# Kernel optimization log

Measured on AMD Instinct MI355X. Metric: run time of the kernel, lower is better.

Reference implementation:

```python
import jax, jax.numpy as jnp
import numpy as np

N1 = 4096
N2 = 4096


def _encoder(x, w1, b1, w2, b2, w3, b3):
    # fc1 -> fc2 -> fc3 -> relu (relu only after fc3, matching the torch code)
    h = x @ w1.T + b1
    h = h @ w2.T + b2
    h = h @ w3.T + b3
    return jax.nn.relu(h)


def _self_attention(x, adj, alpha, W):
    # tmp_i = sum_j [adj_ij==1] * alpha_ij * W * x_j ; tmp_i /= deg_i ; tmp_i += x_i (only if deg_i != 0)
    a = (adj == 1).astype(x.dtype)          # [N, N]
    deg = a.sum(axis=1)                     # [N]
    agg = (a * alpha) @ x                   # [N, 64] masked weighted aggregation
    agg = agg * W[0, 0]
    safe_deg = jnp.maximum(deg, 1.0)
    out = agg / safe_deg[:, None] + x       # residual
    return jnp.where((deg != 0.0)[:, None], out, jnp.zeros_like(out))


def setup_inputs() -> dict:
    key = jax.random.key(0)
    ks = jax.random.split(key, 20)
    s = 0.02  # weight scale to keep activations sane through the 4096->256->128->64 MLP
    inp = {
        "x1": jax.random.normal(ks[0], (N1, N1), jnp.float32),
        "x2": jax.random.normal(ks[1], (N2, N2), jnp.float32),
        "adj1": jax.random.randint(ks[2], (N1, N1), 0, 2, jnp.int32),
        "adj2": jax.random.randint(ks[3], (N2, N2), 0, 2, jnp.int32),
        "e1_w1": jax.random.normal(ks[4], (256, N1), jnp.float32) * s,
        "e1_b1": jnp.zeros((256,), jnp.float32),
        "e1_w2": jax.random.normal(ks[5], (128, 256), jnp.float32) * s,
        "e1_b2": jnp.zeros((128,), jnp.float32),
        "e1_w3": jax.random.normal(ks[6], (64, 128), jnp.float32) * s,
        "e1_b3": jnp.zeros((64,), jnp.float32),
        "e2_w1": jax.random.normal(ks[7], (256, N2), jnp.float32) * s,
        "e2_b1": jnp.zeros((256,), jnp.float32),
        "e2_w2": jax.random.normal(ks[8], (128, 256), jnp.float32) * s,
        "e2_b2": jnp.zeros((128,), jnp.float32),
        "e2_w3": jax.random.normal(ks[9], (64, 128), jnp.float32) * s,
        "e2_b3": jnp.zeros((64,), jnp.float32),
        "W": jax.random.normal(ks[10], (1, 1), jnp.float32),
        "alpha1": jax.random.normal(ks[11], (N1, N1), jnp.float32),
        "clf_w": jax.random.normal(ks[12], (2, (N1 + N2) * 64), jnp.float32) * s,
        "clf_b": jnp.zeros((2,), jnp.float32),
    }
    return inp


def reference(x1, x2, adj1, adj2,
              e1_w1, e1_b1, e1_w2, e1_b2, e1_w3, e1_b3,
              e2_w1, e2_b1, e2_w2, e2_b2, e2_w3, e2_b3,
              W, alpha1, clf_w, clf_b):
    h1 = _encoder(x1, e1_w1, e1_b1, e1_w2, e1_b2, e1_w3, e1_b3)  # [N1, 64]
    h2 = _encoder(x2, e2_w1, e2_b1, e2_w2, e2_b2, e2_w3, e2_b3)  # [N2, 64]
    # NOTE: original torch code uses self.alpha1 for BOTH graphs (alpha2 is unused)
    new1 = _self_attention(h1, adj1, alpha1, W)
    new2 = _self_attention(h2, adj2, alpha1[:N2, :N2], W)
    feat = jnp.concatenate([new1, new2], axis=0).reshape(1, -1)  # [1, (N1+N2)*64]
    return feat @ clf_w.T + clf_b  # [1, 2]
```

## Files before the change

### kernel.cpp

```cpp
#include <hip/hip_runtime.h>
#include <hip/hip_bf16.h>
#include <stdint.h>

#define N 4096

typedef __attribute__((ext_vector_type(4))) float f32x4;
typedef __attribute__((ext_vector_type(8))) short s16x8;

__device__ inline unsigned short f2bf(float f) {
    unsigned int u = __float_as_uint(f);
    u += 0x7fffu + ((u >> 16) & 1u);
    return (unsigned short)(u >> 16);
}
__device__ inline float bf2f(unsigned short h) {
    return __uint_as_float(((unsigned int)h) << 16);
}

__global__ void k0a(const float* __restrict__ w2a, const float* __restrict__ w3a,
                    const float* __restrict__ b1a, const float* __restrict__ b2a, const float* __restrict__ b3a,
                    const float* __restrict__ w2b, const float* __restrict__ w3b,
                    const float* __restrict__ b1b, const float* __restrict__ b2b, const float* __restrict__ b3b,
                    float* __restrict__ T, float* __restrict__ beff) {
    const int g  = blockIdx.x >> 5;
    const int nb = blockIdx.x & 31;
    const float* w2 = g ? w2b : w2a;
    const float* w3 = g ? w3b : w3a;
    const int c  = threadIdx.x;
    const int n0 = nb * 2;
    float a0 = 0.f, a1 = 0.f;
#pragma unroll 8
    for (int r = 0; r < 128; ++r) {
        float w = w2[r * 256 + c];
        a0 += w3[n0 * 128 + r] * w;
        a1 += w3[n0 * 128 + 128 + r] * w;
    }
    float* Tg = T + g * 64 * 256;
    Tg[n0 * 256 + c]       = a0;
    Tg[(n0 + 1) * 256 + c] = a1;

    if (nb == 0) {
        __shared__ float ps[256];
        __shared__ float u[128];
        const float* b1 = g ? b1b : b1a;
        const float* b2 = g ? b2b : b2a;
        const float* b3 = g ? b3b : b3a;
        {
            const int r = threadIdx.x >> 1, half = threadIdx.x & 1;
            float s = 0.f;
#pragma unroll 8
            for (int cc = 0; cc < 128; ++cc) s += w2[r * 256 + half * 128 + cc] * b1[half * 128 + cc];
            ps[threadIdx.x] = s;
        }
        __syncthreads();
        if (threadIdx.x < 128)
            u[threadIdx.x] = ps[2 * threadIdx.x] + ps[2 * threadIdx.x + 1] + b2[threadIdx.x];
        __syncthreads();
        {
            const int n = threadIdx.x >> 2, qr = threadIdx.x & 3;
            float s = 0.f;
#pragma unroll
            for (int r = 0; r < 32; ++r) s += w3[n * 128 + qr * 32 + r] * u[qr * 32 + r];
            ps[threadIdx.x] = s;
        }
        __syncthreads();
        if (threadIdx.x < 64)
            beff[g * 64 + threadIdx.x] = ps[4 * threadIdx.x] + ps[4 * threadIdx.x + 1]
                                       + ps[4 * threadIdx.x + 2] + ps[4 * threadIdx.x + 3] + b3[threadIdx.x];
    }
}

__global__ __launch_bounds__(256) void k0b(const float* __restrict__ w1a, const float* __restrict__ w1b,
                                           const float* __restrict__ T,
                                           unsigned short* __restrict__ Wfrag) {
    const int b  = blockIdx.x;
    const int g = b >> 8, n4 = (b >> 4) & 15, kchunk = b & 15;
    const float* w1 = g ? w1b : w1a;
    const int kx = kchunk * 256 + threadIdx.x;
    const float* Tg = T + (size_t)(g * 64 + n4 * 4) * 256;
    float acc[4] = {0.f, 0.f, 0.f, 0.f};
#pragma unroll 8
    for (int r = 0; r < 256; ++r) {
        float w = w1[(size_t)r * N + kx];
#pragma unroll
        for (int j = 0; j < 4; ++j) acc[j] += Tg[j * 256 + r] * w;
    }
    const int kc = kx >> 6, cc = (kx >> 5) & 1, q = (kx >> 3) & 3, ko = kx & 7;
#pragma unroll
    for (int j = 0; j < 4; ++j) {
        const int n = n4 * 4 + j;
        const int ng = n >> 4, l15 = n & 15;
        const int lane = q * 16 + l15;
        const unsigned short hi = f2bf(acc[j]);
        const unsigned short lo = f2bf(acc[j] - bf2f(hi));
        const size_t unit = ((((size_t)g * 64 + kc) * 4 + ng) * 2 + cc) * 2;
        Wfrag[unit * 512 + lane * 8 + ko]       = hi;
        Wfrag[(unit + 1) * 512 + lane * 8 + ko] = lo;
    }
}

__global__ __launch_bounds__(512, 4) void k1(const float* __restrict__ x1, const float* __restrict__ x2,
                                             const unsigned short* __restrict__ Wfrag,
                                             const float* __restrict__ beff,
                                             float* __restrict__ hf, unsigned short* __restrict__ hfrag) {
    const int b  = blockIdx.x;
    const int g  = b & 1;
    const int i0 = (b >> 1) * 16;
    const float* x = g ? x2 : x1;

    const int t = threadIdx.x;
    const int lane = t & 63, kg = t >> 6;
    const int q = lane >> 4, l15 = lane & 15;

    __shared__ float accs[8][4][64][4];
    __shared__ unsigned short htile[64][16];

    f32x4 acc[4];
#pragma unroll
    for (int ng = 0; ng < 4; ++ng) acc[ng] = (f32x4){0.f, 0.f, 0.f, 0.f};

    const float* xrow = x + (size_t)(i0 + l15) * N;
    for (int kk = 0; kk < 8; ++kk) {
        const int kc = kg * 8 + kk;
#pragma unroll
        for (int c = 0; c < 2; ++c) {
            const int ka = kc * 64 + c * 32 + q * 8;
            float4 a0 = *(const float4*)&xrow[ka];
            float4 a1 = *(const float4*)&xrow[ka + 4];
            s16x8 bh[4], bl[4];
#pragma unroll
            for (int ng = 0; ng < 4; ++ng) {
                const size_t unit = ((((size_t)g * 64 + kc) * 4 + ng) * 2 + c) * 2;
                bh[ng] = *(const s16x8*)&Wfrag[unit * 512 + lane * 8];
                bl[ng] = *(const s16x8*)&Wfrag[(unit + 1) * 512 + lane * 8];
            }
            float xv[8] = {a0.x, a0.y, a0.z, a0.w, a1.x, a1.y, a1.z, a1.w};
            s16x8 ah, al;
#pragma unroll
            for (int j = 0; j < 8; ++j) {
                unsigned short h = f2bf(xv[j]);
                ah[j] = (short)h;
                al[j] = (short)f2bf(xv[j] - bf2f(h));
            }
#pragma unroll
            for (int ng = 0; ng < 4; ++ng) {
                acc[ng] = __builtin_amdgcn_mfma_f32_16x16x32_bf16(al, bh[ng], acc[ng], 0, 0, 0);
                acc[ng] = __builtin_amdgcn_mfma_f32_16x16x32_bf16(ah, bl[ng], acc[ng], 0, 0, 0);
                acc[ng] = __builtin_amdgcn_mfma_f32_16x16x32_bf16(ah, bh[ng], acc[ng], 0, 0, 0);
            }
        }
    }
#pragma unroll
    for (int ng = 0; ng < 4; ++ng)
#pragma unroll
        for (int r = 0; r < 4; ++r) accs[kg][ng][lane][r] = acc[ng][r];
    __syncthreads();

    {
        const int ng = kg & 3, rh = kg >> 2;
        const int n = ng * 16 + l15;
        const float be = beff[g * 64 + n];
#pragma unroll
        for (int rr = 0; rr < 2; ++rr) {
            const int r = rh * 2 + rr;
            float s = 0.f;
#pragma unroll
            for (int k8 = 0; k8 < 8; ++k8) s += accs[k8][ng][lane][r];
            float v = fmaxf(s + be, 0.f);
            const int il = q * 4 + r;
            hf[(size_t)(g * N + i0 + il) * 64 + n] = v;
            htile[n][il] = f2bf(v);
        }
    }
    __syncthreads();

    if (t < 128) {
        const int ng2 = t >> 5, jh = (t >> 4) & 1, l = t & 15;
        uint4 v = *(const uint4*)&htile[ng2 * 16 + l][jh * 8];
        const int jc = i0 >> 6, c = (i0 >> 5) & 1, q0 = (i0 >> 3) & 3;
        const size_t unit = (((size_t)g * 4 + ng2) * 64 + jc) * 2 + c;
        *(uint4*)&hfrag[unit * 512 + (size_t)(q0 + jh) * 128 + l * 8] = v;
    }
}

__global__ __launch_bounds__(512, 2) void k2(const int* __restrict__ adj1, const int* __restrict__ adj2,
                                             const float* __restrict__ alpha,
                                             const unsigned short* __restrict__ hfrag,
                                             float* __restrict__ pagg, float* __restrict__ pdeg) {
    const int b  = blockIdx.x;
    const int ks = b & 3;
    const int i0 = (b >> 2) * 16;
    const int t = threadIdx.x;
    const int lane = t & 63, kg = t >> 6;
    const int q = lane >> 4, l15 = lane & 15;

    __shared__ float accs[8][4][64][4];
    __shared__ float degp[8][64][2];

    f32x4 acc1[4], acc2[4];
#pragma unroll
    for (int ng = 0; ng < 4; ++ng) {
        acc1[ng] = (f32x4){0.f, 0.f, 0.f, 0.f};
        acc2[ng] = (f32x4){0.f, 0.f, 0.f, 0.f};
    }
    int deg1 = 0, deg2 = 0;

    const size_t rowoff = (size_t)(i0 + l15) * N;
    for (int kk = 0; kk < 2; ++kk) {
        const int jc = ks * 16 + kg * 2 + kk;
#pragma unroll
        for (int c = 0; c < 2; ++c) {
            const int ka = jc * 64 + c * 32 + q * 8;
            const size_t ao = rowoff + ka;
            float4 a0 = *(const float4*)&alpha[ao];
            float4 a1 = *(const float4*)&alpha[ao + 4];
            int4 j10 = *(const int4*)&adj1[ao];
            int4 j11 = *(const int4*)&adj1[ao + 4];
            int4 j20 = *(const int4*)&adj2[ao];
            int4 j21 = *(const int4*)&adj2[ao + 4];
            s16x8 ha1[4], ha2[4];
#pragma unroll
            for (int ng = 0; ng < 4; ++ng) {
                const size_t u1 = (((size_t)0 * 4 + ng) * 64 + jc) * 2 + c;
                const size_t u2 = (((size_t)1 * 4 + ng) * 64 + jc) * 2 + c;
                ha1[ng] = *(const s16x8*)&hfrag[u1 * 512 + lane * 8];
                ha2[ng] = *(const s16x8*)&hfrag[u2 * 512 + lane * 8];
            }
            float av[8] = {a0.x, a0.y, a0.z, a0.w, a1.x, a1.y, a1.z, a1.w};
            int m1[8] = {j10.x == 1, j10.y == 1, j10.z == 1, j10.w == 1,
                         j11.x == 1, j11.y == 1, j11.z == 1, j11.w == 1};
            int m2[8] = {j20.x == 1, j20.y == 1, j20.z == 1, j20.w == 1,
                         j21.x == 1, j21.y == 1, j21.z == 1, j21.w == 1};
            s16x8 bf1, bf2;
#pragma unroll
            for (int j = 0; j < 8; ++j) {
                short bv = (short)f2bf(av[j]);
                bf1[j] = m1[j] ? bv : (short)0;
                bf2[j] = m2[j] ? bv : (short)0;
                deg1 += m1[j];
                deg2 += m2[j];
            }
#pragma unroll
            for (int ng = 0; ng < 4; ++ng) {
                acc1[ng] = __builtin_amdgcn_mfma_f32_16x16x32_bf16(ha1[ng], bf1, acc1[ng], 0, 0, 0);
                acc2[ng] = __builtin_amdgcn_mfma_f32_16x16x32_bf16(ha2[ng], bf2, acc2[ng], 0, 0, 0);
            }
        }
    }

    degp[kg][lane][0] = (float)deg1;
    degp[kg][lane][1] = (float)deg2;
#pragma unroll
    for (int ng = 0; ng < 4; ++ng)
#pragma unroll
        for (int r = 0; r < 4; ++r) accs[kg][ng][lane][r] = acc1[ng][r];
    __syncthreads();
    if (t < 32) {
        int gg = t >> 4, row = t & 15;
        float s = 0.f;
#pragma unroll
        for (int w = 0; w < 8; ++w)
#pragma unroll
            for (int qq = 0; qq < 4; ++qq) s += degp[w][qq * 16 + row][gg];
        pdeg[(size_t)(gg * 4 + ks) * 4096 + i0 + row] = s;
    }

    {
        const int ng = kg & 3, rh = kg >> 2;
        const int i = i0 + l15;
#pragma unroll
        for (int rr = 0; rr < 2; ++rr) {
            const int r = rh * 2 + rr;
            float s = 0.f;
#pragma unroll
            for (int k8 = 0; k8 < 8; ++k8) s += accs[k8][ng][lane][r];
            const int n = ng * 16 + q * 4 + r;
            pagg[(((size_t)ks * 4096 + i) << 6) + n] = s;
        }
    }
    __syncthreads();
#pragma unroll
    for (int ng = 0; ng < 4; ++ng)
#pragma unroll
        for (int r = 0; r < 4; ++r) accs[kg][ng][lane][r] = acc2[ng][r];
    __syncthreads();
    {
        const int ng = kg & 3, rh = kg >> 2;
        const int i = i0 + l15;
#pragma unroll
        for (int rr = 0; rr < 2; ++rr) {
            const int r = rh * 2 + rr;
            float s = 0.f;
#pragma unroll
            for (int k8 = 0; k8 < 8; ++k8) s += accs[k8][ng][lane][r];
            const int n = ng * 16 + q * 4 + r;
            pagg[(((size_t)(4 + ks) * 4096 + i) << 6) + n] = s;
        }
    }
}

__global__ __launch_bounds__(256) void k2b(const float* __restrict__ pagg, const float* __restrict__ pdeg,
                                           const float* __restrict__ hf, const float* __restrict__ Wp,
                                           float* __restrict__ outv) {
    const int idx = blockIdx.x * 256 + threadIdx.x;
    const int gi  = idx >> 4;
    const int nq  = idx & 15;
    const int g   = gi >> 12, i = gi & 4095;
    const float W00 = Wp[0];

    float dg = 0.f;
#pragma unroll
    for (int ks = 0; ks < 4; ++ks) dg += pdeg[(size_t)(g * 4 + ks) * 4096 + i];

    f32x4 s = (f32x4){0.f, 0.f, 0.f, 0.f};
#pragma unroll
    for (int ks = 0; ks < 4; ++ks) {
        const f32x4 p = *(const f32x4*)&pagg[(((size_t)(g * 4 + ks) * 4096 + i) << 6) + nq * 4];
        s += p;
    }
    const f32x4 hv = *(const f32x4*)&hf[((size_t)gi << 6) + nq * 4];
    const float dmax = fmaxf(dg, 1.f);
    f32x4 o;
#pragma unroll
    for (int j = 0; j < 4; ++j)
        o[j] = (dg != 0.f) ? (s[j] * W00 / dmax + hv[j]) : 0.f;
    *(f32x4*)&outv[((size_t)gi << 6) + nq * 4] = o;
}

__global__ __launch_bounds__(256) void k3a(const float* __restrict__ feat, const float* __restrict__ clfw,
                                           float* __restrict__ part) {
    const int t = threadIdx.x;
    const size_t idx = (size_t)blockIdx.x * 2048 + (size_t)t * 8;
    float4 a0 = *(const float4*)&feat[idx];
    float4 a1 = *(const float4*)&feat[idx + 4];
    float4 c0 = *(const float4*)&clfw[idx];
    float4 c1 = *(const float4*)&clfw[idx + 4];
    float4 d0 = *(const float4*)&clfw[524288 + idx];
    float4 d1 = *(const float4*)&clfw[524288 + idx + 4];
    float s0 = a0.x * c0.x + a0.y * c0.y + a0.z * c0.z + a0.w * c0.w
             + a1.x * c1.x + a1.y * c1.y + a1.z * c1.z + a1.w * c1.w;
    float s1 = a0.x * d0.x + a0.y * d0.y + a0.z * d0.z + a0.w * d0.w
             + a1.x * d1.x + a1.y * d1.y + a1.z * d1.z + a1.w * d1.w;
    __shared__ float r0[256], r1[256];
    r0[t] = s0; r1[t] = s1;
    __syncthreads();
    for (int s = 128; s > 0; s >>= 1) {
        if (t < s) { r0[t] += r0[t + s]; r1[t] += r1[t + s]; }
        __syncthreads();
    }
    if (t == 0) { part[blockIdx.x * 2] = r0[0]; part[blockIdx.x * 2 + 1] = r1[0]; }
}

__global__ void k3b(const float* __restrict__ part, const float* __restrict__ clfb,
                    float* __restrict__ outp) {
    const int t = threadIdx.x;
    __shared__ float r0[256], r1[256];
    r0[t] = part[t * 2]; r1[t] = part[t * 2 + 1];
    __syncthreads();
    for (int s = 128; s > 0; s >>= 1) {
        if (t < s) { r0[t] += r0[t + s]; r1[t] += r1[t + s]; }
        __syncthreads();
    }
    if (t == 0) { outp[0] = r0[0] + clfb[0]; outp[1] = r1[0] + clfb[1]; }
}

extern "C" void kernel_launch(void* const* d_in, const int* in_sizes, int n_in,
                              void* d_out, int out_size, void* d_ws, size_t ws_size,
                              hipStream_t stream) {
    const float* x1   = (const float*)d_in[0];
    const float* x2   = (const float*)d_in[1];
    const int*   adj1 = (const int*)d_in[2];
    const int*   adj2 = (const int*)d_in[3];
    const float* e1w1 = (const float*)d_in[4];
    const float* e1b1 = (const float*)d_in[5];
    const float* e1w2 = (const float*)d_in[6];
    const float* e1b2 = (const float*)d_in[7];
    const float* e1w3 = (const float*)d_in[8];
    const float* e1b3 = (const float*)d_in[9];
    const float* e2w1 = (const float*)d_in[10];
    const float* e2b1 = (const float*)d_in[11];
    const float* e2w2 = (const float*)d_in[12];
    const float* e2b2 = (const float*)d_in[13];
    const float* e2w3 = (const float*)d_in[14];
    const float* e2b3 = (const float*)d_in[15];
    const float* Wp   = (const float*)d_in[16];
    const float* alph = (const float*)d_in[17];
    const float* clfw = (const float*)d_in[18];
    const float* clfb = (const float*)d_in[19];

    char* wsb = (char*)d_ws;
    unsigned short* Wfrag = (unsigned short*)(wsb);
    float* newv = (float*)(wsb);
    unsigned short* hfrag = (unsigned short*)(wsb + (2u << 20));
    float* hf   = (float*)(wsb + (3u << 20));
    float* T    = (float*)(wsb + (5u << 20));
    float* beff = (float*)(wsb + (5u << 20) + (1u << 17));
    float* part = (float*)(wsb + (5u << 20) + (1u << 17) + 4096);
    float* pagg = (float*)(wsb + (6u << 20));
    float* pdeg = (float*)(wsb + (14u << 20));

    hipLaunchKernelGGL(k0a, dim3(64), dim3(256), 0, stream,
                       e1w2, e1w3, e1b1, e1b2, e1b3, e2w2, e2w3, e2b1, e2b2, e2b3, T, beff);
    hipLaunchKernelGGL(k0b, dim3(512), dim3(256), 0, stream, e1w1, e2w1, T, Wfrag);
    hipLaunchKernelGGL(k1, dim3(512), dim3(512), 0, stream, x1, x2, Wfrag, beff, hf, hfrag);
    hipLaunchKernelGGL(k2, dim3(1024), dim3(512), 0, stream, adj1, adj2, alph, hfrag, pagg, pdeg);
    hipLaunchKernelGGL(k2b, dim3(512), dim3(256), 0, stream, pagg, pdeg, hf, Wp, newv);
    hipLaunchKernelGGL(k3a, dim3(256), dim3(256), 0, stream, newv, clfw, part);
    hipLaunchKernelGGL(k3b, dim3(1), dim3(256), 0, stream, part, clfb, (float*)d_out);
}
```

Before: 400.9 us.

## Stage adj/alpha tiles through swizzled LDS with coalesced row loads and double buffering

The k2 aggregation kernel now has each thread load contiguous 8-element row segments of alpha/adj1/adj2 (32 threads per row) so global reads are coalesced. The masked bf16 values go into a double-buffered, XOR-swizzled LDS tile, and MFMA operands are read back from LDS while the next stage's global loads are in flight. Block-index remapping also pairs adjacent row tiles for the same k-split, which may improve L2 locality on hfrag. The cost is extra LDS traffic and a barrier per stage, and the accs scratch now aliases the staging buffer.

```diff
diff --git a/kernel.cpp b/kernel.cpp
--- a/kernel.cpp
+++ b/kernel.cpp
@@ -187,14 +187,15 @@
                                              const unsigned short* __restrict__ hfrag,
                                              float* __restrict__ pagg, float* __restrict__ pdeg) {
     const int b  = blockIdx.x;
-    const int ks = b & 3;
-    const int i0 = (b >> 2) * 16;
+    const int ks = (b >> 1) & 3;
+    const int i0 = ((((b >> 3) << 1) | (b & 1))) << 4;
     const int t = threadIdx.x;
     const int lane = t & 63, kg = t >> 6;
     const int q = lane >> 4, l15 = lane & 15;
 
-    __shared__ float accs[8][4][64][4];
-    __shared__ float degp[8][64][2];
+    __shared__ __align__(16) unsigned short am[2][2][16][256];
+    __shared__ float degp[2][16][32];
+    float (*accs)[4][64][4] = reinterpret_cast<float (*)[4][64][4]>(&am[0][0][0][0]);
 
     f32x4 acc1[4], acc2[4];
 #pragma unroll
@@ -204,63 +205,83 @@
     }
     int deg1 = 0, deg2 = 0;
 
-    const size_t rowoff = (size_t)(i0 + l15) * N;
-    for (int kk = 0; kk < 2; ++kk) {
-        const int jc = ks * 16 + kg * 2 + kk;
-#pragma unroll
-        for (int c = 0; c < 2; ++c) {
-            const int ka = jc * 64 + c * 32 + q * 8;
-            const size_t ao = rowoff + ka;
-            float4 a0 = *(const float4*)&alpha[ao];
-            float4 a1 = *(const float4*)&alpha[ao + 4];
-            int4 j10 = *(const int4*)&adj1[ao];
-            int4 j11 = *(const int4*)&adj1[ao + 4];
-            int4 j20 = *(const int4*)&adj2[ao];
-            int4 j21 = *(const int4*)&adj2[ao + 4];
-            s16x8 ha1[4], ha2[4];
-#pragma unroll
-            for (int ng = 0; ng < 4; ++ng) {
-                const size_t u1 = (((size_t)0 * 4 + ng) * 64 + jc) * 2 + c;
-                const size_t u2 = (((size_t)1 * 4 + ng) * 64 + jc) * 2 + c;
-                ha1[ng] = *(const s16x8*)&hfrag[u1 * 512 + lane * 8];
-                ha2[ng] = *(const s16x8*)&hfrag[u2 * 512 + lane * 8];
-            }
-            float av[8] = {a0.x, a0.y, a0.z, a0.w, a1.x, a1.y, a1.z, a1.w};
-            int m1[8] = {j10.x == 1, j10.y == 1, j10.z == 1, j10.w == 1,
-                         j11.x == 1, j11.y == 1, j11.z == 1, j11.w == 1};
-            int m2[8] = {j20.x == 1, j20.y == 1, j20.z == 1, j20.w == 1,
-                         j21.x == 1, j21.y == 1, j21.z == 1, j21.w == 1};
-            s16x8 bf1, bf2;
-#pragma unroll
-            for (int j = 0; j < 8; ++j) {
-                short bv = (short)f2bf(av[j]);
-                bf1[j] = m1[j] ? bv : (short)0;
-                bf2[j] = m2[j] ? bv : (short)0;
-                deg1 += m1[j];
-                deg2 += m2[j];
-            }
-#pragma unroll
-            for (int ng = 0; ng < 4; ++ng) {
-                acc1[ng] = __builtin_amdgcn_mfma_f32_16x16x32_bf16(ha1[ng], bf1, acc1[ng], 0, 0, 0);
-                acc2[ng] = __builtin_amdgcn_mfma_f32_16x16x32_bf16(ha2[ng], bf2, acc2[ng], 0, 0, 0);
-            }
-        }
-    }
-
-    degp[kg][lane][0] = (float)deg1;
-    degp[kg][lane][1] = (float)deg2;
+    const int srow = t >> 5, scg = t & 31;
+    const size_t sbase = (size_t)(i0 + srow) * N + (size_t)ks * 1024 + (size_t)scg * 8;
+    char* const amb = (char*)&am[0][0][0][0];
+    const int swoff = (srow * 512 + scg * 16) ^ ((srow & 7) << 4);
+    const int rdoff = (l15 * 512 + kg * 64 + q * 16) ^ ((l15 & 7) << 4);
+
+    float4 sa0, sa1; int4 sj10, sj11, sj20, sj21;
+
+#define K2_ISSUE(S) do { \
+        const float* ap = alpha + sbase + (S) * 256; \
+        sa0 = *(const float4*)ap; sa1 = *(const float4*)(ap + 4); \
+        const int* p1 = adj1 + sbase + (S) * 256; \
+        sj10 = *(const int4*)p1; sj11 = *(const int4*)(p1 + 4); \
+        const int* p2 = adj2 + sbase + (S) * 256; \
+        sj20 = *(const int4*)p2; sj21 = *(const int4*)(p2 + 4); \
+    } while (0)
+
+#define K2_CONVSTORE(BUF) do { \
+        float av[8] = {sa0.x, sa0.y, sa0.z, sa0.w, sa1.x, sa1.y, sa1.z, sa1.w}; \
+        int m1[8] = {sj10.x == 1, sj10.y == 1, sj10.z == 1, sj10.w == 1, \
+                     sj11.x == 1, sj11.y == 1, sj11.z == 1, sj11.w == 1}; \
+        int m2[8] = {sj20.x == 1, sj20.y == 1, sj20.z == 1, sj20.w == 1, \
+                     sj21.x == 1, sj21.y == 1, sj21.z == 1, sj21.w == 1}; \
+        s16x8 w1v, w2v; \
+        _Pragma("unroll") \
+        for (int j = 0; j < 8; ++j) { \
+            unsigned short bv = f2bf(av[j]); \
+            w1v[j] = m1[j] ? (short)bv : (short)0; \
+            w2v[j] = m2[j] ? (short)bv : (short)0; \
+            deg1 += m1[j]; deg2 += m2[j]; \
+        } \
+        *(s16x8*)(amb + (BUF) * 16384 + swoff) = w1v; \
+        *(s16x8*)(amb + (BUF) * 16384 + 8192 + swoff) = w2v; \
+    } while (0)
+
+#define K2_COMPUTE(S) do { \
+        const int jc = ks * 16 + (S) * 4 + (kg >> 1), cph = kg & 1; \
+        s16x8 ha1[4], ha2[4]; \
+        _Pragma("unroll") \
+        for (int ng = 0; ng < 4; ++ng) { \
+            const size_t u1 = (((size_t)ng) * 64 + jc) * 2 + cph; \
+            const size_t u2 = (((size_t)(4 + ng)) * 64 + jc) * 2 + cph; \
+            ha1[ng] = *(const s16x8*)&hfrag[u1 * 512 + lane * 8]; \
+            ha2[ng] = *(const s16x8*)&hfrag[u2 * 512 + lane * 8]; \
+        } \
+        s16x8 bfa = *(const s16x8*)(amb + ((S) & 1) * 16384 + rdoff); \
+        s16x8 bfb = *(const s16x8*)(amb + ((S) & 1) * 16384 + 8192 + rdoff); \
+        _Pragma("unroll") \
+        for (int ng = 0; ng < 4; ++ng) { \
+            acc1[ng] = __builtin_amdgcn_mfma_f32_16x16x32_bf16(ha1[ng], bfa, acc1[ng], 0, 0, 0); \
+            acc2[ng] = __builtin_amdgcn_mfma_f32_16x16x32_bf16(ha2[ng], bfb, acc2[ng], 0, 0, 0); \
+        } \
+    } while (0)
+
+    K2_ISSUE(0);
+    K2_CONVSTORE(0);
+    __syncthreads();
+#pragma unroll
+    for (int s = 0; s < 4; ++s) {
+        if (s < 3) K2_ISSUE(s + 1);
+        K2_COMPUTE(s);
+        if (s < 3) K2_CONVSTORE((s + 1) & 1);
+        __syncthreads();
+    }
+
+    degp[0][srow][scg] = (float)deg1;
+    degp[1][srow][scg] = (float)deg2;
 #pragma unroll
     for (int ng = 0; ng < 4; ++ng)
 #pragma unroll
         for (int r = 0; r < 4; ++r) accs[kg][ng][lane][r] = acc1[ng][r];
     __syncthreads();
     if (t < 32) {
-        int gg = t >> 4, row = t & 15;
+        const int gg = t >> 4, row = t & 15;
         float s = 0.f;
 #pragma unroll
-        for (int w = 0; w < 8; ++w)
-#pragma unroll
-            for (int qq = 0; qq < 4; ++qq) s += degp[w][qq * 16 + row][gg];
+        for (int c2 = 0; c2 < 32; ++c2) s += degp[gg][row][c2];
         pdeg[(size_t)(gg * 4 + ks) * 4096 + i0 + row] = s;
     }
 
@@ -296,6 +317,9 @@
             pagg[(((size_t)(4 + ks) * 4096 + i) << 6) + n] = s;
         }
     }
+#undef K2_ISSUE
+#undef K2_CONVSTORE
+#undef K2_COMPUTE
 }
 
 __global__ __launch_bounds__(256) void k2b(const float* __restrict__ pagg, const float* __restrict__ pdeg,
```

Result: no change. 395.0 us (-1.5%).
